# Kernel tuning notes

Measured on AMD Instinct MI355X. Metric: run time of the kernel, lower is better.

Reference implementation:

```python
import jax, jax.numpy as jnp
import numpy as np

H = 32      # num attention heads
HD = 64     # head dim
RD = 16     # rotary dim = 0.25 * head_dim (partial rotary)
EPS = 1e-5
BASE = 10000.0


def _ln(x, w, b):
    m = x.mean(-1, keepdims=True)
    v = ((x - m) ** 2).mean(-1, keepdims=True)
    return (x - m) / jnp.sqrt(v + EPS) * w + b


def _rot_half(x):
    x1, x2 = jnp.split(x, 2, axis=-1)
    return jnp.concatenate([-x2, x1], axis=-1)


def setup_inputs() -> dict:
    key = jax.random.key(0)
    ks = jax.random.split(key, 16)
    B, S, D, FF = 1, 2048, 2048, 8192
    std = 0.02
    hidden_states = jax.random.normal(ks[0], (B, S, D), jnp.float32)
    memory = jax.random.normal(ks[1], (B, S, D), jnp.float32)
    # causal additive mask (B,1,S,S): 0 where allowed, -inf above diagonal
    causal = jnp.where(jnp.tril(jnp.ones((S, S), bool)), 0.0, -jnp.inf).astype(jnp.float32)
    attention_mask = jnp.broadcast_to(causal[None, None], (B, 1, S, S))
    position_ids = jnp.broadcast_to(jnp.arange(S, dtype=jnp.int32), (B, S))
    return {
        'hidden_states': hidden_states,
        'memory': memory,
        'attention_mask': attention_mask,
        'position_ids': position_ids,
        'ln1_w': jnp.ones((D,), jnp.float32),
        'ln1_b': jnp.zeros((D,), jnp.float32),
        'ln2_w': jnp.ones((D,), jnp.float32),
        'ln2_b': jnp.zeros((D,), jnp.float32),
        'Wq': jax.random.normal(ks[2], (D, D), jnp.float32) * std,
        'Wk': jax.random.normal(ks[3], (D, D), jnp.float32) * std,
        'Wv': jax.random.normal(ks[4], (D, D), jnp.float32) * std,
        'Wo': jax.random.normal(ks[5], (D, D), jnp.float32) * std,
        'Wg': jax.random.normal(ks[6], (FF, D), jnp.float32) * std,
        'Wu': jax.random.normal(ks[7], (FF, D), jnp.float32) * std,
        'Wd': jax.random.normal(ks[8], (D, FF), jnp.float32) * std,
    }


def reference(hidden_states, memory, attention_mask, position_ids,
              ln1_w, ln1_b, ln2_w, ln2_b, Wq, Wk, Wv, Wo, Wg, Wu, Wd):
    B, S, D = hidden_states.shape
    residual = hidden_states
    h = _ln(hidden_states, ln1_w, ln1_b)
    mem = _ln(memory, ln1_w, ln1_b)

    # fast_forward: concat memory in front along sequence
    x = jnp.concatenate([mem, h], axis=1)              # (B, 2S, D)
    pos = jnp.concatenate([position_ids, position_ids], axis=1)  # (B, 2S)
    L = 2 * S

    q = (x @ Wq.T).reshape(B, L, H, HD).transpose(0, 2, 1, 3)  # (B,H,2S,HD)
    k = (x @ Wk.T).reshape(B, L, H, HD).transpose(0, 2, 1, 3)
    v = (x @ Wv.T).reshape(B, L, H, HD).transpose(0, 2, 1, 3)

    # partial rotary embedding
    inv_freq = 1.0 / (BASE ** (jnp.arange(0, RD, 2, dtype=jnp.float32) / RD))
    t = pos.astype(jnp.float32)[:, :, None] * inv_freq       # (B,2S,RD/2)
    emb = jnp.concatenate([t, t], axis=-1)                   # (B,2S,RD)
    cos = jnp.cos(emb)[:, None]                              # (B,1,2S,RD)
    sin = jnp.sin(emb)[:, None]
    qr, qp = q[..., :RD], q[..., RD:]
    kr, kp = k[..., :RD], k[..., RD:]
    qr = qr * cos + _rot_half(qr) * sin
    kr = kr * cos + _rot_half(kr) * sin
    q = jnp.concatenate([qr, qp], axis=-1)
    k = jnp.concatenate([kr, kp], axis=-1)

    # only non-memory queries attend
    q = q[:, :, S:]                                          # (B,H,S,HD)
    scores = jnp.einsum('bhqd,bhkd->bhqk', q, k) / jnp.sqrt(jnp.float32(HD))  # (B,H,S,2S)

    # left mask: causal + no attending to own memory slot; right: only own position (+ causal)
    eye = jnp.eye(S, dtype=bool)[None, None]
    left = jnp.where(eye, -jnp.inf, attention_mask)
    right = jnp.where(eye, attention_mask, -jnp.inf)
    mask = jnp.concatenate([left, right], axis=-1)           # (B,1,S,2S)

    w = jax.nn.softmax((scores + mask).astype(jnp.float32), axis=-1).astype(q.dtype)
    attn = jnp.einsum('bhqk,bhkd->bhqd', w, v)
    attn = attn.transpose(0, 2, 1, 3).reshape(B, S, D) @ Wo.T

    h = residual + attn
    residual2 = h
    h2 = _ln(h, ln2_w, ln2_b)
    mlp = (jax.nn.silu(h2 @ Wg.T) * (h2 @ Wu.T)) @ Wd.T
    return residual2 + mlp
```

## Files before the change

kernel.cpp:

```cpp
#include <hip/hip_runtime.h>
#include <stdint.h>
#include <stddef.h>

typedef short s16;
typedef __attribute__((ext_vector_type(8))) short short8;
typedef __attribute__((ext_vector_type(4))) float float4v;

#define S_LEN 2048
#define DMODEL 2048
#define LLEN 4096
#define FFDIM 8192
#define NHEAD 32
#define HDIM 64

#define AS1 __attribute__((address_space(1)))
#define AS3 __attribute__((address_space(3)))

__device__ __forceinline__ float bf2f(short s) {
  union { uint32_t u; float f; } x;
  x.u = ((uint32_t)(uint16_t)s) << 16;
  return x.f;
}
__device__ __forceinline__ short f2bf(float f) {
  union { float f; uint32_t u; } x;
  x.f = f;
  uint32_t r = x.u + 0x7fffu + ((x.u >> 16) & 1u);
  return (short)(r >> 16);
}

template <typename T> __device__ __forceinline__ float ldv(const T* p, size_t i);
template <> __device__ __forceinline__ float ldv<float>(const float* p, size_t i) { return p[i]; }
template <> __device__ __forceinline__ float ldv<s16>(const s16* p, size_t i) { return bf2f(p[i]); }
template <typename T> __device__ __forceinline__ void stv(T* p, size_t i, float v);
template <> __device__ __forceinline__ void stv<float>(float* p, size_t i, float v) { p[i] = v; }
template <> __device__ __forceinline__ void stv<s16>(s16* p, size_t i, float v) { p[i] = f2bf(v); }

__global__ __launch_bounds__(256) void w2bf(const float* __restrict__ src, s16* __restrict__ dst,
                                            int n8) {
  const int i = blockIdx.x * 256 + threadIdx.x;
  if (i >= n8) return;
  const float4v a = ((const float4v*)src)[2 * i];
  const float4v b = ((const float4v*)src)[2 * i + 1];
  short8 o;
#pragma unroll
  for (int j = 0; j < 4; j++) { o[j] = f2bf(a[j]); o[j + 4] = f2bf(b[j]); }
  ((short8*)dst)[i] = o;
}

template <typename T>
__global__ __launch_bounds__(256) void ln_kernel(const T* __restrict__ src,
                                                 const float* __restrict__ w,
                                                 const float* __restrict__ b,
                                                 s16* __restrict__ dst) {
  const int row = blockIdx.x, t = threadIdx.x;
  float v[8];
  float s = 0.f, s2 = 0.f;
#pragma unroll
  for (int i = 0; i < 8; i++) {
    v[i] = ldv<T>(src, (size_t)row * DMODEL + t * 8 + i);
    s += v[i];
    s2 += v[i] * v[i];
  }
#pragma unroll
  for (int off = 32; off > 0; off >>= 1) {
    s += __shfl_down(s, off);
    s2 += __shfl_down(s2, off);
  }
  __shared__ float rs[4], rs2[4];
  if ((t & 63) == 0) { rs[t >> 6] = s; rs2[t >> 6] = s2; }
  __syncthreads();
  const float fs = rs[0] + rs[1] + rs[2] + rs[3];
  const float fs2 = rs2[0] + rs2[1] + rs2[2] + rs2[3];
  const float mean = fs * (1.f / (float)DMODEL);
  const float var = fs2 * (1.f / (float)DMODEL) - mean * mean;
  const float rstd = rsqrtf(var + 1e-5f);
  const float4v w0 = *(const float4v*)(w + t * 8);
  const float4v w1 = *(const float4v*)(w + t * 8 + 4);
  const float4v b0 = *(const float4v*)(b + t * 8);
  const float4v b1 = *(const float4v*)(b + t * 8 + 4);
  short8 o;
#pragma unroll
  for (int i = 0; i < 4; i++) {
    o[i] = f2bf((v[i] - mean) * rstd * w0[i] + b0[i]);
    o[i + 4] = f2bf((v[i + 4] - mean) * rstd * w1[i] + b1[i]);
  }
  *(short8*)(dst + (size_t)row * DMODEL + t * 8) = o;
}

__global__ __launch_bounds__(256) void init_out(float4v* __restrict__ dst,
                                                const float4v* __restrict__ src, int n4) {
  const int i = blockIdx.x * 256 + threadIdx.x;
  if (i < n4) dst[i] = src ? src[i] : float4v{0.f, 0.f, 0.f, 0.f};
}

template <typename T>
__global__ __launch_bounds__(256) void rope_kernel(T* __restrict__ buf, const int* __restrict__ pos,
                                                   int nrows) {
  const int idx = blockIdx.x * 256 + threadIdx.x;
  if (idx >= nrows * NHEAD) return;
  const int row = idx >> 5, h = idx & 31;
  const int pid = pos[row < S_LEN ? row : row - S_LEN];
  T* ptr = buf + (size_t)row * DMODEL + h * HDIM;
  float a[8], c[8];
  if constexpr (sizeof(T) == 2) {
    const short8 r0 = *(const short8*)ptr;
    const short8 r1 = *(const short8*)(ptr + 8);
#pragma unroll
    for (int f = 0; f < 8; f++) { a[f] = bf2f(r0[f]); c[f] = bf2f(r1[f]); }
  } else {
    const float4v x0 = *(const float4v*)ptr;
    const float4v x1 = *(const float4v*)(ptr + 4);
    const float4v x2 = *(const float4v*)(ptr + 8);
    const float4v x3 = *(const float4v*)(ptr + 12);
#pragma unroll
    for (int f = 0; f < 4; f++) { a[f] = x0[f]; a[f + 4] = x1[f]; c[f] = x2[f]; c[f + 4] = x3[f]; }
  }
  const float inv_freq[8] = {1.0f, 0.31622776601683794f, 0.1f, 0.031622776601683794f,
                             0.01f, 0.0031622776601683794f, 0.001f, 0.00031622776601683794f};
  const float fp = (float)pid;
  float o0[8], o1[8];
#pragma unroll
  for (int f = 0; f < 8; f++) {
    float sv, cv;
    sincosf(fp * inv_freq[f], &sv, &cv);
    o0[f] = a[f] * cv - c[f] * sv;
    o1[f] = c[f] * cv + a[f] * sv;
  }
  if constexpr (sizeof(T) == 2) {
    short8 w0, w1;
#pragma unroll
    for (int f = 0; f < 8; f++) { w0[f] = f2bf(o0[f]); w1[f] = f2bf(o1[f]); }
    *(short8*)ptr = w0;
    *(short8*)(ptr + 8) = w1;
  } else {
    float4v y0, y1, y2, y3;
#pragma unroll
    for (int f = 0; f < 4; f++) { y0[f] = o0[f]; y1[f] = o0[f + 4]; y2[f] = o1[f]; y3[f] = o1[f + 4]; }
    *(float4v*)ptr = y0;
    *(float4v*)(ptr + 4) = y1;
    *(float4v*)(ptr + 8) = y2;
    *(float4v*)(ptr + 12) = y3;
  }
}

template <int EPI, int BSRC, typename AUXT, typename OUTT>
__global__ __launch_bounds__(256) void gemm_bt(const s16* __restrict__ A, const void* __restrict__ Wp,
                                               OUTT* __restrict__ C, const AUXT* __restrict__ aux,
                                               int M, int N, int K) {
  __shared__ alignas(16) s16 As[128 * 32];
  __shared__ alignas(16) s16 Bs[128 * 32];
  const int t = threadIdx.x;
  const int wave = t >> 6, lane = t & 63;
  const int quad = lane >> 4, l15 = lane & 15;
  const int n0 = blockIdx.x * 128, m0 = blockIdx.y * 128;
  const int wm = wave >> 1, wn = wave & 1;
  const int srow = lane >> 2, skk = (lane & 3) * 8;
  const int br4 = t >> 2, bc4 = (t & 3) * 8;
  const int kchunk = K / (int)gridDim.z;
  const int kbeg = kchunk * (int)blockIdx.z;

  float4v acc[4][4];
#pragma unroll
  for (int i = 0; i < 4; i++)
#pragma unroll
    for (int j = 0; j < 4; j++) acc[i][j] = float4v{0.f, 0.f, 0.f, 0.f};

  const float* wrow0 = (const float*)Wp + (size_t)(n0 + br4) * K + bc4;
  const float* wrow1 = wrow0 + (size_t)64 * K;
  const s16* Wb = (const s16*)Wp;

  for (int k0 = kbeg; k0 < kbeg + kchunk; k0 += 32) {
    if constexpr (BSRC == 0) {
      float4v wa0 = *(const float4v*)(wrow0 + k0);
      float4v wa1 = *(const float4v*)(wrow0 + k0 + 4);
      float4v wb0 = *(const float4v*)(wrow1 + k0);
      float4v wb1 = *(const float4v*)(wrow1 + k0 + 4);
      __syncthreads();
#pragma unroll
      for (int cc = 0; cc < 2; cc++) {
        const int ci = wave * 2 + cc;
        const s16* ga = A + (size_t)(m0 + ci * 16 + srow) * K + (k0 + skk);
        __builtin_amdgcn_global_load_lds((const AS1 void*)ga, (AS3 void*)(&As[ci * 512]), 16, 0, 0);
      }
      short8 c0, c1;
#pragma unroll
      for (int i = 0; i < 4; i++) {
        c0[i] = f2bf(wa0[i]);
        c0[i + 4] = f2bf(wa1[i]);
        c1[i] = f2bf(wb0[i]);
        c1[i + 4] = f2bf(wb1[i]);
      }
      *(short8*)&Bs[br4 * 32 + bc4] = c0;
      *(short8*)&Bs[(64 + br4) * 32 + bc4] = c1;
    } else {
      __syncthreads();
#pragma unroll
      for (int cc = 0; cc < 2; cc++) {
        const int ci = wave * 2 + cc;
        const s16* ga = A + (size_t)(m0 + ci * 16 + srow) * K + (k0 + skk);
        __builtin_amdgcn_global_load_lds((const AS1 void*)ga, (AS3 void*)(&As[ci * 512]), 16, 0, 0);
        const s16* gb = Wb + (size_t)(n0 + ci * 16 + srow) * K + (k0 + skk);
        __builtin_amdgcn_global_load_lds((const AS1 void*)gb, (AS3 void*)(&Bs[ci * 512]), 16, 0, 0);
      }
    }
    __syncthreads();
    short8 a[4], b[4];
#pragma unroll
    for (int mt = 0; mt < 4; mt++)
      a[mt] = *(const short8*)&As[(wm * 64 + mt * 16 + l15) * 32 + quad * 8];
#pragma unroll
    for (int nt = 0; nt < 4; nt++)
      b[nt] = *(const short8*)&Bs[(wn * 64 + nt * 16 + l15) * 32 + quad * 8];
#pragma unroll
    for (int mt = 0; mt < 4; mt++)
#pragma unroll
      for (int nt = 0; nt < 4; nt++)
        acc[mt][nt] = __builtin_amdgcn_mfma_f32_16x16x32_bf16(a[mt], b[nt], acc[mt][nt], 0, 0, 0);
  }
#pragma unroll
  for (int mt = 0; mt < 4; mt++) {
#pragma unroll
    for (int nt = 0; nt < 4; nt++) {
      const float* av = (const float*)&acc[mt][nt];
      const int col = n0 + wn * 64 + nt * 16 + l15;
      const int rowb = m0 + wm * 64 + mt * 16 + quad * 4;
#pragma unroll
      for (int r = 0; r < 4; r++) {
        const size_t idx = (size_t)(rowb + r) * N + col;
        float v = av[r];
        if constexpr (EPI == 3) {
          unsafeAtomicAdd((float*)&C[idx], v);
        } else {
          if (EPI == 1) v += ldv<AUXT>(aux, idx);
          if (EPI == 2) { const float g = ldv<AUXT>(aux, idx); v *= g / (1.0f + __expf(-g)); }
          stv<OUTT>(C, idx, v);
        }
      }
    }
  }
}

__global__ __launch_bounds__(256) void attn_kernel(const float* __restrict__ qb, const s16* __restrict__ kb,
                                                   const s16* __restrict__ vb, s16* __restrict__ attn) {
  __shared__ alignas(16) s16 Qs[64 * 72];
  __shared__ alignas(16) s16 Ks[64 * 72];
  __shared__ alignas(16) s16 Vt[64 * 72];
  __shared__ alignas(16) s16 Ps[64 * 72];
  const int t = threadIdx.x;
  const int h = blockIdx.x & 31;
  const int qblk = 31 - (int)(blockIdx.x >> 5);
  const int wave = t >> 6, lane = t & 63;
  const int quad = lane >> 4, l15 = lane & 15;

#pragma unroll
  for (int rr = 0; rr < 2; rr++) {
    const int tt = t + rr * 256;
    const int i = tt >> 3, d0 = (tt & 7) * 8;
    const float* qp = qb + (size_t)(qblk * 64 + i) * DMODEL + h * HDIM + d0;
    const float4v q0 = *(const float4v*)qp;
    const float4v q1 = *(const float4v*)(qp + 4);
    short8 o;
#pragma unroll
    for (int x = 0; x < 4; x++) { o[x] = f2bf(q0[x]); o[x + 4] = f2bf(q1[x]); }
    *(short8*)&Qs[i * 72 + d0] = o;
  }

  float4v O[4];
#pragma unroll
  for (int i = 0; i < 4; i++) O[i] = float4v{0.f, 0.f, 0.f, 0.f};
  float m_run[4] = {-1e30f, -1e30f, -1e30f, -1e30f};
  float l_run[4] = {0.f, 0.f, 0.f, 0.f};

  const int nchunks = qblk + 2;
  for (int c = 0; c < nchunks; ++c) {
    const int krow = (c <= qblk) ? c * 64 : (S_LEN + qblk * 64);
    __syncthreads();
#pragma unroll
    for (int rr = 0; rr < 2; rr++) {
      const int tt = t + rr * 256;
      const int j = tt >> 3, d0 = (tt & 7) * 8;
      *(short8*)&Ks[j * 72 + d0] =
          *(const short8*)(kb + (size_t)(krow + j) * DMODEL + h * HDIM + d0);
      const short8 vv = *(const short8*)(vb + (size_t)(krow + j) * DMODEL + h * HDIM + d0);
#pragma unroll
      for (int x = 0; x < 8; x++) Vt[(d0 + x) * 72 + j] = vv[x];
    }
    __syncthreads();

    float4v Sacc[4];
#pragma unroll
    for (int i = 0; i < 4; i++) Sacc[i] = float4v{0.f, 0.f, 0.f, 0.f};
#pragma unroll
    for (int ks = 0; ks < 2; ks++) {
      const short8 af = *(const short8*)&Qs[(wave * 16 + l15) * 72 + ks * 32 + quad * 8];
#pragma unroll
      for (int nt = 0; nt < 4; nt++) {
        const short8 bf = *(const short8*)&Ks[(nt * 16 + l15) * 72 + ks * 32 + quad * 8];
        Sacc[nt] = __builtin_amdgcn_mfma_f32_16x16x32_bf16(af, bf, Sacc[nt], 0, 0, 0);
      }
    }
    float* sp = (float*)Sacc;
#pragma unroll
    for (int nt = 0; nt < 4; nt++)
#pragma unroll
      for (int r = 0; r < 4; r++) {
        const int il = wave * 16 + quad * 4 + r;
        const int jl = nt * 16 + l15;
        bool ok;
        if (c < qblk) ok = true;
        else if (c == qblk) ok = (jl < il);
        else ok = (jl == il);
        sp[nt * 4 + r] = ok ? fminf(sp[nt * 4 + r] * 0.125f, 1e4f) : -1e30f;
      }
#pragma unroll
    for (int r = 0; r < 4; r++) {
      float mx = fmaxf(fmaxf(sp[0 * 4 + r], sp[1 * 4 + r]), fmaxf(sp[2 * 4 + r], sp[3 * 4 + r]));
#pragma unroll
      for (int off = 1; off < 16; off <<= 1) mx = fmaxf(mx, __shfl_xor(mx, off));
      const float mnew = fmaxf(m_run[r], mx);
      float alpha, sum;
      if (mnew < -1e29f) {
        alpha = 1.f; sum = 0.f;
#pragma unroll
        for (int nt = 0; nt < 4; nt++) sp[nt * 4 + r] = 0.f;
      } else {
        alpha = __expf(m_run[r] - mnew);
        m_run[r] = mnew;
        sum = 0.f;
#pragma unroll
        for (int nt = 0; nt < 4; nt++) {
          const float p = __expf(sp[nt * 4 + r] - mnew);
          sp[nt * 4 + r] = p;
          sum += p;
        }
      }
#pragma unroll
      for (int off = 1; off < 16; off <<= 1) sum += __shfl_xor(sum, off);
      l_run[r] = l_run[r] * alpha + sum;
      float* op = (float*)O;
#pragma unroll
      for (int dt = 0; dt < 4; dt++) op[dt * 4 + r] *= alpha;
    }
#pragma unroll
    for (int nt = 0; nt < 4; nt++)
#pragma unroll
      for (int r = 0; r < 4; r++)
        Ps[(wave * 16 + quad * 4 + r) * 72 + nt * 16 + l15] = f2bf(sp[nt * 4 + r]);
#pragma unroll
    for (int ks = 0; ks < 2; ks++) {
      const short8 pf = *(const short8*)&Ps[(wave * 16 + l15) * 72 + ks * 32 + quad * 8];
#pragma unroll
      for (int dt = 0; dt < 4; dt++) {
        const short8 vf = *(const short8*)&Vt[(dt * 16 + l15) * 72 + ks * 32 + quad * 8];
        O[dt] = __builtin_amdgcn_mfma_f32_16x16x32_bf16(pf, vf, O[dt], 0, 0, 0);
      }
    }
  }
  const float* op = (const float*)O;
#pragma unroll
  for (int dt = 0; dt < 4; dt++)
#pragma unroll
    for (int r = 0; r < 4; r++) {
      const int row = qblk * 64 + wave * 16 + quad * 4 + r;
      const int col = h * HDIM + dt * 16 + l15;
      const float inv_l = 1.0f / fmaxf(l_run[r], 1e-20f);
      attn[(size_t)row * DMODEL + col] = f2bf(op[dt * 4 + r] * inv_l);
    }
}

extern "C" void kernel_launch(void* const* d_in, const int* in_sizes, int n_in,
                              void* d_out, int out_size, void* d_ws, size_t ws_size,
                              hipStream_t stream) {
  const float* hidden = (const float*)d_in[0];
  const float* memory = (const float*)d_in[1];
  const int* pos_ids = (const int*)d_in[3];
  const float* ln1_w = (const float*)d_in[4];
  const float* ln1_b = (const float*)d_in[5];
  const float* ln2_w = (const float*)d_in[6];
  const float* ln2_b = (const float*)d_in[7];
  const float* Wq = (const float*)d_in[8];
  const float* Wk = (const float*)d_in[9];
  const float* Wv = (const float*)d_in[10];
  const float* Wo = (const float*)d_in[11];
  const float* Wg = (const float*)d_in[12];
  const float* Wu = (const float*)d_in[13];
  const float* Wd = (const float*)d_in[14];
  s16* ws = (s16*)d_ws;
  const size_t M1 = (size_t)1024 * 1024;

  s16* x = ws;
  float* q = (float*)d_out;
  s16* k = ws + 8 * M1;
  s16* v = ws + 16 * M1;
  s16* attn = ws;
  s16* h2 = ws + 4 * M1;
  s16* g = ws + 8 * M1;

  const bool bw = ws_size >= (size_t)88 * M1 * sizeof(s16);
  s16* Wqb = ws + 24 * M1;
  s16* Wkb = Wqb + 4 * M1;
  s16* Wvb = Wkb + 4 * M1;
  s16* Wob = Wvb + 4 * M1;
  s16* Wgb = Wob + 4 * M1;
  s16* Wub = Wgb + 16 * M1;
  s16* Wdb = Wub + 16 * M1;

  if (bw) {
    w2bf<<<2048, 256, 0, stream>>>(Wq, Wqb, 512 * 1024);
    w2bf<<<2048, 256, 0, stream>>>(Wk, Wkb, 512 * 1024);
    w2bf<<<2048, 256, 0, stream>>>(Wv, Wvb, 512 * 1024);
    w2bf<<<2048, 256, 0, stream>>>(Wo, Wob, 512 * 1024);
    w2bf<<<8192, 256, 0, stream>>>(Wg, Wgb, 2048 * 1024);
    w2bf<<<8192, 256, 0, stream>>>(Wu, Wub, 2048 * 1024);
    w2bf<<<8192, 256, 0, stream>>>(Wd, Wdb, 2048 * 1024);
  }

  ln_kernel<float><<<S_LEN, 256, 0, stream>>>(memory, ln1_w, ln1_b, x);
  ln_kernel<float><<<S_LEN, 256, 0, stream>>>(hidden, ln1_w, ln1_b, x + (size_t)S_LEN * DMODEL);
  init_out<<<4096, 256, 0, stream>>>((float4v*)d_out, (const float4v*)nullptr, 1 << 20);
  if (bw) {
    gemm_bt<3, 1, float, float><<<dim3(16, 16, 4), 256, 0, stream>>>(x + (size_t)S_LEN * DMODEL, Wqb, q, (const float*)nullptr, S_LEN, DMODEL, DMODEL);
    gemm_bt<0, 1, s16, s16><<<dim3(16, 32), 256, 0, stream>>>(x, Wkb, k, (const s16*)nullptr, LLEN, DMODEL, DMODEL);
    gemm_bt<0, 1, s16, s16><<<dim3(16, 32), 256, 0, stream>>>(x, Wvb, v, (const s16*)nullptr, LLEN, DMODEL, DMODEL);
  } else {
    gemm_bt<3, 0, float, float><<<dim3(16, 16, 4), 256, 0, stream>>>(x + (size_t)S_LEN * DMODEL, Wq, q, (const float*)nullptr, S_LEN, DMODEL, DMODEL);
    gemm_bt<0, 0, s16, s16><<<dim3(16, 32), 256, 0, stream>>>(x, Wk, k, (const s16*)nullptr, LLEN, DMODEL, DMODEL);
    gemm_bt<0, 0, s16, s16><<<dim3(16, 32), 256, 0, stream>>>(x, Wv, v, (const s16*)nullptr, LLEN, DMODEL, DMODEL);
  }
  rope_kernel<float><<<(S_LEN * NHEAD) / 256, 256, 0, stream>>>(q, pos_ids, S_LEN);
  rope_kernel<s16><<<(LLEN * NHEAD) / 256, 256, 0, stream>>>(k, pos_ids, LLEN);
  attn_kernel<<<NHEAD * (S_LEN / 64), 256, 0, stream>>>(q, k, v, attn);
  init_out<<<4096, 256, 0, stream>>>((float4v*)d_out, (const float4v*)hidden, 1 << 20);
  if (bw)
    gemm_bt<3, 1, float, float><<<dim3(16, 16, 4), 256, 0, stream>>>(attn, Wob, (float*)d_out, (const float*)nullptr, S_LEN, DMODEL, DMODEL);
  else
    gemm_bt<3, 0, float, float><<<dim3(16, 16, 4), 256, 0, stream>>>(attn, Wo, (float*)d_out, (const float*)nullptr, S_LEN, DMODEL, DMODEL);
  ln_kernel<float><<<S_LEN, 256, 0, stream>>>((const float*)d_out, ln2_w, ln2_b, h2);
  if (bw) {
    gemm_bt<0, 1, s16, s16><<<dim3(64, 16), 256, 0, stream>>>(h2, Wgb, g, (const s16*)nullptr, S_LEN, FFDIM, DMODEL);
    gemm_bt<2, 1, s16, s16><<<dim3(64, 16), 256, 0, stream>>>(h2, Wub, g, g, S_LEN, FFDIM, DMODEL);
    gemm_bt<3, 1, float, float><<<dim3(16, 16, 4), 256, 0, stream>>>(g, Wdb, (float*)d_out, (const float*)nullptr, S_LEN, DMODEL, FFDIM);
  } else {
    gemm_bt<0, 0, s16, s16><<<dim3(64, 16), 256, 0, stream>>>(h2, Wg, g, (const s16*)nullptr, S_LEN, FFDIM, DMODEL);
    gemm_bt<2, 0, s16, s16><<<dim3(64, 16), 256, 0, stream>>>(h2, Wu, g, g, S_LEN, FFDIM, DMODEL);
    gemm_bt<3, 0, float, float><<<dim3(16, 16, 4), 256, 0, stream>>>(g, Wd, (float*)d_out, (const float*)nullptr, S_LEN, DMODEL, FFDIM);
  }
}
```

Before: 1.057 ms.

## Prefetch K/V into registers, swizzle V transpose, use exp2 softmax in attention

The attention kernel now loads the next chunk's K/V tiles into registers while the current chunk computes, replacing the synchronous global-to-LDS load at the top of each iteration. The V transpose store into shared memory is XOR-swizzled to reduce bank conflicts, and the read side uses the same swizzle. The softmax folds log2(e) into the scale and uses exp2f, and unmasked chunks skip the per-element mask logic. s_setprio hints are placed around the MFMA blocks. The gain depends on how much of the attention kernel's time goes to memory latency versus the large GEMMs elsewhere, and the raw barriers must keep the LDS reuse correct.

```diff
diff --git a/kernel.cpp b/kernel.cpp
--- a/kernel.cpp
+++ b/kernel.cpp
@@ -271,25 +271,44 @@
   float m_run[4] = {-1e30f, -1e30f, -1e30f, -1e30f};
   float l_run[4] = {0.f, 0.f, 0.f, 0.f};
 
+  const float SCALE = 0.125f * 1.442695040888963f;
+
+  const int j0 = t >> 3, d00 = (t & 7) * 8;
+  const int vkeyw = (d00 >> 3) & 7;
+  const size_t colb = (size_t)h * HDIM + d00;
+
   const int nchunks = qblk + 2;
+  short8 kr0 = *(const short8*)(kb + (size_t)j0 * DMODEL + colb);
+  short8 kr1 = *(const short8*)(kb + (size_t)(j0 + 32) * DMODEL + colb);
+  short8 vr0 = *(const short8*)(vb + (size_t)j0 * DMODEL + colb);
+  short8 vr1 = *(const short8*)(vb + (size_t)(j0 + 32) * DMODEL + colb);
+
   for (int c = 0; c < nchunks; ++c) {
-    const int krow = (c <= qblk) ? c * 64 : (S_LEN + qblk * 64);
-    __syncthreads();
-#pragma unroll
-    for (int rr = 0; rr < 2; rr++) {
-      const int tt = t + rr * 256;
-      const int j = tt >> 3, d0 = (tt & 7) * 8;
-      *(short8*)&Ks[j * 72 + d0] =
-          *(const short8*)(kb + (size_t)(krow + j) * DMODEL + h * HDIM + d0);
-      const short8 vv = *(const short8*)(vb + (size_t)(krow + j) * DMODEL + h * HDIM + d0);
-#pragma unroll
-      for (int x = 0; x < 8; x++) Vt[(d0 + x) * 72 + j] = vv[x];
-    }
-    __syncthreads();
+    asm volatile("s_waitcnt lgkmcnt(0)" ::: "memory");
+    __builtin_amdgcn_s_barrier();
+    asm volatile("" ::: "memory");
+    *(short8*)&Ks[j0 * 72 + d00] = kr0;
+    *(short8*)&Ks[(j0 + 32) * 72 + d00] = kr1;
+#pragma unroll
+    for (int x = 0; x < 8; x++) {
+      Vt[(d00 + x) * 72 + (j0 ^ (vkeyw << 3))] = vr0[x];
+      Vt[(d00 + x) * 72 + ((j0 + 32) ^ (vkeyw << 3))] = vr1[x];
+    }
+    if (c + 1 < nchunks) {
+      const int krow = (c + 1 <= qblk) ? (c + 1) * 64 : (S_LEN + qblk * 64);
+      kr0 = *(const short8*)(kb + (size_t)(krow + j0) * DMODEL + colb);
+      kr1 = *(const short8*)(kb + (size_t)(krow + j0 + 32) * DMODEL + colb);
+      vr0 = *(const short8*)(vb + (size_t)(krow + j0) * DMODEL + colb);
+      vr1 = *(const short8*)(vb + (size_t)(krow + j0 + 32) * DMODEL + colb);
+    }
+    asm volatile("s_waitcnt lgkmcnt(0)" ::: "memory");
+    __builtin_amdgcn_s_barrier();
+    asm volatile("" ::: "memory");
 
     float4v Sacc[4];
 #pragma unroll
     for (int i = 0; i < 4; i++) Sacc[i] = float4v{0.f, 0.f, 0.f, 0.f};
+    __builtin_amdgcn_s_setprio(1);
 #pragma unroll
     for (int ks = 0; ks < 2; ks++) {
       const short8 af = *(const short8*)&Qs[(wave * 16 + l15) * 72 + ks * 32 + quad * 8];
@@ -299,19 +318,22 @@
         Sacc[nt] = __builtin_amdgcn_mfma_f32_16x16x32_bf16(af, bf, Sacc[nt], 0, 0, 0);
       }
     }
+    __builtin_amdgcn_s_setprio(0);
     float* sp = (float*)Sacc;
-#pragma unroll
-    for (int nt = 0; nt < 4; nt++)
-#pragma unroll
-      for (int r = 0; r < 4; r++) {
-        const int il = wave * 16 + quad * 4 + r;
-        const int jl = nt * 16 + l15;
-        bool ok;
-        if (c < qblk) ok = true;
-        else if (c == qblk) ok = (jl < il);
-        else ok = (jl == il);
-        sp[nt * 4 + r] = ok ? fminf(sp[nt * 4 + r] * 0.125f, 1e4f) : -1e30f;
-      }
+    if (c < qblk) {
+#pragma unroll
+      for (int i = 0; i < 16; i++) sp[i] = fminf(sp[i] * SCALE, 2e4f);
+    } else {
+#pragma unroll
+      for (int nt = 0; nt < 4; nt++)
+#pragma unroll
+        for (int r = 0; r < 4; r++) {
+          const int il = wave * 16 + quad * 4 + r;
+          const int jl = nt * 16 + l15;
+          const bool ok = (c == qblk) ? (jl < il) : (jl == il);
+          sp[nt * 4 + r] = ok ? fminf(sp[nt * 4 + r] * SCALE, 2e4f) : -1e30f;
+        }
+    }
 #pragma unroll
     for (int r = 0; r < 4; r++) {
       float mx = fmaxf(fmaxf(sp[0 * 4 + r], sp[1 * 4 + r]), fmaxf(sp[2 * 4 + r], sp[3 * 4 + r]));
@@ -324,12 +346,12 @@
 #pragma unroll
         for (int nt = 0; nt < 4; nt++) sp[nt * 4 + r] = 0.f;
       } else {
-        alpha = __expf(m_run[r] - mnew);
+        alpha = exp2f(m_run[r] - mnew);
         m_run[r] = mnew;
         sum = 0.f;
 #pragma unroll
         for (int nt = 0; nt < 4; nt++) {
-          const float p = __expf(sp[nt * 4 + r] - mnew);
+          const float p = exp2f(sp[nt * 4 + r] - mnew);
           sp[nt * 4 + r] = p;
           sum += p;
         }
@@ -346,15 +368,19 @@
 #pragma unroll
       for (int r = 0; r < 4; r++)
         Ps[(wave * 16 + quad * 4 + r) * 72 + nt * 16 + l15] = f2bf(sp[nt * 4 + r]);
+    __builtin_amdgcn_s_setprio(1);
 #pragma unroll
     for (int ks = 0; ks < 2; ks++) {
       const short8 pf = *(const short8*)&Ps[(wave * 16 + l15) * 72 + ks * 32 + quad * 8];
 #pragma unroll
       for (int dt = 0; dt < 4; dt++) {
-        const short8 vf = *(const short8*)&Vt[(dt * 16 + l15) * 72 + ks * 32 + quad * 8];
+        const int dd = dt * 16 + l15;
+        const int vkey = (dd >> 3) & 7;
+        const short8 vf = *(const short8*)&Vt[dd * 72 + ((ks * 32 + quad * 8) ^ (vkey << 3))];
         O[dt] = __builtin_amdgcn_mfma_f32_16x16x32_bf16(pf, vf, O[dt], 0, 0, 0);
       }
     }
+    __builtin_amdgcn_s_setprio(0);
   }
   const float* op = (const float*)O;
 #pragma unroll
```

Result: faster. 1.015 ms (-3.9%).
